# Performance work log

Hardware: AMD Instinct MI355X
Metric: run time of the kernel (lower is better)

## Reference

```python
import jax, jax.numpy as jnp
import numpy as np

B, S, D = 2, 2048, 2048
H, HK, HD = 16, 4, 128          # query heads, kv heads, head dim (H*HD == D)
HID = 4 * D                      # SwiGLU hidden (mult=4)
WIN, SINK = 1024, 4              # sliding window, attention sink tokens
EPS = 1e-6
ROPE_BASE = 10000.0


def rmsnorm(x, g):
    return x * jax.lax.rsqrt(jnp.mean(x * x, axis=-1, keepdims=True) + EPS) * g


def rope_tables(seq_len, head_dim):
    inv = 1.0 / (ROPE_BASE ** (jnp.arange(0, head_dim, 2, dtype=jnp.float32) / head_dim))
    ang = jnp.arange(seq_len, dtype=jnp.float32)[:, None] * inv[None, :]  # [S, HD/2]
    return jnp.cos(ang), jnp.sin(ang)


def apply_rope(x, cos, sin):
    # x: [B, S, h, HD]; rotate-half convention
    x1, x2 = jnp.split(x, 2, axis=-1)
    c = cos[None, :, None, :]
    s = sin[None, :, None, :]
    return jnp.concatenate([x1 * c - x2 * s, x2 * c + x1 * s], axis=-1)


def setup_inputs() -> dict:
    key = jax.random.key(0)
    ks = jax.random.split(key, 10)
    p = 0.02
    return {
        "x": jax.random.normal(ks[0], (B, S, D), dtype=jnp.float32),
        "g1": jnp.ones((D,), dtype=jnp.float32),
        "g2": jnp.ones((D,), dtype=jnp.float32),
        "wq": jax.random.normal(ks[1], (D, H * HD), dtype=jnp.float32) * p,
        "wk": jax.random.normal(ks[2], (D, HK * HD), dtype=jnp.float32) * p,
        "wv": jax.random.normal(ks[3], (D, HK * HD), dtype=jnp.float32) * p,
        "wo": jax.random.normal(ks[4], (H * HD, D), dtype=jnp.float32) * p,
        "w_gate": jax.random.normal(ks[5], (D, HID), dtype=jnp.float32) * p,
        "w_up": jax.random.normal(ks[6], (D, HID), dtype=jnp.float32) * p,
        "w_down": jax.random.normal(ks[7], (HID, D), dtype=jnp.float32) * p,
    }


def reference(x, g1, g2, wq, wk, wv, wo, w_gate, w_up, w_down):
    # ---- pre-norm attention ----
    h = rmsnorm(x, g1)
    q = (h @ wq).reshape(B, S, H, HD)
    k = (h @ wk).reshape(B, S, HK, HD)
    v = (h @ wv).reshape(B, S, HK, HD)

    cos, sin = rope_tables(S, HD)
    q = apply_rope(q, cos, sin)
    k = apply_rope(k, cos, sin)

    # GQA: expand kv heads to query heads
    rep = H // HK
    k = jnp.repeat(k, rep, axis=2)  # [B, S, H, HD]
    v = jnp.repeat(v, rep, axis=2)

    scores = jnp.einsum("bqhd,bkhd->bhqk", q, k) / jnp.sqrt(jnp.float32(HD))

    # causal + sliding-window + attention-sink mask
    i = jnp.arange(S)[:, None]
    j = jnp.arange(S)[None, :]
    allowed = (j <= i) & (((i - j) < WIN) | (j < SINK))  # [S, S]
    scores = jnp.where(allowed[None, None], scores, jnp.float32(-1e9))

    attn = jax.nn.softmax(scores, axis=-1)
    a = jnp.einsum("bhqk,bkhd->bqhd", attn, v).reshape(B, S, H * HD) @ wo

    x = x + a

    # ---- pre-norm SwiGLU FFN ----
    h2 = rmsnorm(x, g2)
    ffn = (jax.nn.silu(h2 @ w_gate) * (h2 @ w_up)) @ w_down
    return x + ffn
```

## Files before the change

kernel.cpp:

```cpp
#include <hip/hip_runtime.h>
#include <hip/hip_bf16.h>
#include <stdint.h>

#define TOK 4096
#define SEQ 2048
#define DM 2048
#define NH 16
#define NKV 4
#define HDIM 128
#define HID 8192
#define WIN 1024
#define SINKN 4

typedef float f32x4 __attribute__((ext_vector_type(4)));
typedef __bf16 bf16x8 __attribute__((ext_vector_type(8)));
typedef unsigned short u16;
typedef unsigned int u32;

#define VM(n) asm volatile("s_waitcnt vmcnt(" #n ")" ::: "memory")
#define LG(n) asm volatile("s_waitcnt lgkmcnt(" #n ")" ::: "memory")
#define SCHED0 __builtin_amdgcn_sched_barrier(0)

__device__ __forceinline__ u16 f2bf(float f) {
  union { float f; u32 u; } v; v.f = f;
  return (u16)((v.u + 0x7fffu + ((v.u >> 16) & 1u)) >> 16);
}
__device__ __forceinline__ float bf2f(u16 h) {
  union { u32 u; float f; } v; v.u = ((u32)h) << 16;
  return v.f;
}
__device__ __forceinline__ f32x4 mfma16(bf16x8 a, bf16x8 b, f32x4 c) {
  return __builtin_amdgcn_mfma_f32_16x16x32_bf16(a, b, c, 0, 0, 0);
}
__device__ __forceinline__ void gld16(const u16* g, u16* l) {
  __builtin_amdgcn_global_load_lds(
      (const __attribute__((address_space(1))) u32*)g,
      (__attribute__((address_space(3))) u32*)l, 16, 0, 0);
}
__device__ __forceinline__ void bar() {
  asm volatile("s_barrier" ::: "memory");
}
__device__ __forceinline__ void swz_rc(int c, int& row, int& k8) {
  row = 2 * (c >> 3) + (((c >> 2) & 1) ^ ((c >> 4) & 1));
  k8 = (c & 3) ^ (row & 3);
}
__device__ __forceinline__ void raster8(int wg, int nwg, int nbx, int& bx, int& by) {
  int cpx = nwg >> 3;
  int s = (wg & 7) * cpx + (wg >> 3);
  by = 8 * (s / (8 * nbx)) + (s & 7);
  bx = (s >> 3) % nbx;
}

__global__ __launch_bounds__(256)
void wtrans_all(const float* __restrict__ wq, const float* __restrict__ wk,
                const float* __restrict__ wv, const float* __restrict__ wo,
                const float* __restrict__ wg, const float* __restrict__ wu,
                const float* __restrict__ wd,
                u16* __restrict__ dqkv, u16* __restrict__ dwo,
                u16* __restrict__ dwg, u16* __restrict__ dwu,
                u16* __restrict__ dwd)
{
  int id = blockIdx.x;
  const float* src; u16* dst; int K, N, lgn;
  if (id < 4096)       { src = wq; dst = dqkv;                        K = 2048; N = 2048; lgn = 6; }
  else if (id < 5120)  { id -= 4096;  src = wk; dst = dqkv + (size_t)DM * DM;          K = 2048; N = 512;  lgn = 4; }
  else if (id < 6144)  { id -= 5120;  src = wv; dst = dqkv + (size_t)(DM + 512) * DM;  K = 2048; N = 512;  lgn = 4; }
  else if (id < 10240) { id -= 6144;  src = wo; dst = dwo;            K = 2048; N = 2048; lgn = 6; }
  else if (id < 26624) { id -= 10240; src = wg; dst = dwg;            K = 2048; N = 8192; lgn = 8; }
  else if (id < 43008) { id -= 26624; src = wu; dst = dwu;            K = 2048; N = 8192; lgn = 8; }
  else                 { id -= 43008; src = wd; dst = dwd;            K = 8192; N = 2048; lgn = 6; }
  int bx = id & ((1 << lgn) - 1);
  int by = id >> lgn;

  __shared__ float t[32][33];
  int tx = threadIdx.x & 31, ty = threadIdx.x >> 5;
  #pragma unroll
  for (int i = 0; i < 4; i++) {
    int r = ty + i * 8;
    t[r][tx] = src[(size_t)(by * 32 + r) * N + bx * 32 + tx];
  }
  __syncthreads();
  #pragma unroll
  for (int i = 0; i < 4; i++) {
    int r = ty + i * 8;
    dst[(size_t)(bx * 32 + r) * K + by * 32 + tx] = f2bf(t[tx][r]);
  }
}

__global__ __launch_bounds__(256)
void vtrans(const u16* __restrict__ in, int ld, u16* __restrict__ out)
{
  __shared__ u16 t[32][33];
  int tx = threadIdx.x & 31, ty = threadIdx.x >> 5;
  int bx = blockIdx.x;
  int by = blockIdx.y;
  #pragma unroll
  for (int i = 0; i < 4; i++) {
    int r = ty + i * 8;
    t[r][tx] = in[(size_t)(by * 32 + r) * ld + bx * 32 + tx];
  }
  __syncthreads();
  int b = (by * 32) >> 11;
  int s0 = (by * 32) & (SEQ - 1);
  #pragma unroll
  for (int i = 0; i < 4; i++) {
    int c = bx * 32 + ty + i * 8;
    out[(size_t)(b * (NKV * HDIM) + c) * SEQ + s0 + tx] = t[tx][ty + i * 8];
  }
}

__global__ __launch_bounds__(256)
void rope_table_k(float* __restrict__ ct, float* __restrict__ st)
{
  int idx = blockIdx.x * 256 + threadIdx.x;
  int pos = idx >> 6, d = idx & 63;
  float inv = powf(10000.0f, -(float)d / 64.0f);
  float a = (float)pos * inv;
  ct[idx] = cosf(a);
  st[idx] = sinf(a);
}

__global__ void rope_apply_k(u16* __restrict__ q, int ld,
                             const float* __restrict__ ct,
                             const float* __restrict__ st, float scale)
{
  int t = blockIdx.x;
  int hh = threadIdx.x >> 6;
  int d = threadIdx.x & 63;
  int pos = t & (SEQ - 1);
  size_t base = (size_t)t * ld + hh * HDIM + d;
  float x1 = bf2f(q[base]), x2 = bf2f(q[base + 64]);
  float c = ct[pos * 64 + d], s = st[pos * 64 + d];
  q[base]      = f2bf((x1 * c - x2 * s) * scale);
  q[base + 64] = f2bf((x2 * c + x1 * s) * scale);
}

__global__ __launch_bounds__(256)
void rmsnorm_k(const float* __restrict__ x, const float* __restrict__ g,
               u16* __restrict__ o)
{
  int row = blockIdx.x;
  int tid = threadIdx.x;
  const float* xr = x + (size_t)row * DM;
  float4 v0 = *(const float4*)(xr + tid * 8);
  float4 v1 = *(const float4*)(xr + tid * 8 + 4);
  float ss = v0.x*v0.x + v0.y*v0.y + v0.z*v0.z + v0.w*v0.w
           + v1.x*v1.x + v1.y*v1.y + v1.z*v1.z + v1.w*v1.w;
  #pragma unroll
  for (int d = 1; d < 64; d <<= 1) ss += __shfl_xor(ss, d);
  __shared__ float red[4];
  if ((tid & 63) == 0) red[tid >> 6] = ss;
  __syncthreads();
  float inv = rsqrtf((red[0] + red[1] + red[2] + red[3]) * (1.0f / DM) + 1e-6f);
  float4 g0 = *(const float4*)(g + tid * 8);
  float4 g1 = *(const float4*)(g + tid * 8 + 4);
  ushort4 o0, o1;
  o0.x = f2bf(v0.x * inv * g0.x); o0.y = f2bf(v0.y * inv * g0.y);
  o0.z = f2bf(v0.z * inv * g0.z); o0.w = f2bf(v0.w * inv * g0.w);
  o1.x = f2bf(v1.x * inv * g1.x); o1.y = f2bf(v1.y * inv * g1.y);
  o1.z = f2bf(v1.z * inv * g1.z); o1.w = f2bf(v1.w * inv * g1.w);
  *(ushort4*)(o + (size_t)row * DM + tid * 8) = o0;
  *(ushort4*)(o + (size_t)row * DM + tid * 8 + 4) = o1;
}

template<int EPI>
__global__ __launch_bounds__(512, 1)
void gemmp(const u16* __restrict__ A, const u16* __restrict__ Bt,
           u16* __restrict__ Cb, float* __restrict__ Cf,
           const float* __restrict__ X, int M, int N, int K, int nbx)
{
  constexpr int ASZ = 128 * 64;
  constexpr int SLOT = ASZ + 256 * 64;
  __shared__ u16 lds[3 * SLOT];

  int bx, by;
  raster8(blockIdx.x, gridDim.x, nbx, bx, by);
  int m0 = by * 128;
  int n0 = bx * 256;

  int tid = threadIdx.x;
  int l = tid & 63, w = tid >> 6;
  int l16 = l & 15, lg = l >> 4;
  int wr = w >> 2, wc = w & 3;

  int aoff[4][2], boff[4][2];
  #pragma unroll
  for (int m = 0; m < 4; m++)
    #pragma unroll
    for (int kk = 0; kk < 2; kk++) {
      int row = wr * 64 + m * 16 + l16;
      aoff[m][kk] = ((row * 128 + kk * 64 + lg * 16) ^ ((row & 7) << 4)) >> 1;
    }
  #pragma unroll
  for (int n = 0; n < 4; n++)
    #pragma unroll
    for (int kk = 0; kk < 2; kk++) {
      int br = wc * 64 + n * 16 + l16;
      boff[n][kk] = ASZ + (((br * 128 + kk * 64 + lg * 16) ^ ((br & 7) << 4)) >> 1);
    }

  int urow = tid >> 3;
  int cc = (tid & 7) ^ (urow & 7);
  const u16* pA[2];
  const u16* pB[4];
  pA[0] = A + (size_t)(m0 + urow) * K + cc * 8;
  pA[1] = A + (size_t)(m0 + 64 + urow) * K + cc * 8;
  #pragma unroll
  for (int u = 0; u < 4; u++)
    pB[u] = Bt + (size_t)(n0 + u * 64 + urow) * K + cc * 8;

  const int NT = K >> 6;

  auto stA = [&](int tt, int u) {
    gld16(pA[u] + (size_t)tt * 64, lds + (tt % 3) * SLOT + u * 4096 + tid * 8);
  };
  auto stB = [&](int tt, int u) {
    gld16(pB[u] + (size_t)tt * 64, lds + (tt % 3) * SLOT + ASZ + u * 4096 + tid * 8);
  };

  #pragma unroll
  for (int u = 0; u < 4; u++) stB(0, u);
  stA(0, 0); stA(0, 1);
  #pragma unroll
  for (int u = 0; u < 4; u++) stB(1, u);
  stA(1, 0); stA(1, 1);
  VM(6);
  bar();

  f32x4 acc[4][4];
  f32x4 zero = {0.f, 0.f, 0.f, 0.f};
  #pragma unroll
  for (int m = 0; m < 4; m++)
    #pragma unroll
    for (int n = 0; n < 4; n++) acc[m][n] = zero;

  for (int t = 0; t < NT; ++t) {
    u16* cur = lds + (t % 3) * SLOT;
    const bool st = (t + 2 < NT);

    if (st) { stB(t + 2, 0); stB(t + 2, 1); stB(t + 2, 2); }
    bf16x8 a[4][2], b[2][2], c2[2][2];
    #pragma unroll
    for (int m = 0; m < 4; m++) {
      a[m][0] = *(const bf16x8*)(cur + aoff[m][0]);
      a[m][1] = *(const bf16x8*)(cur + aoff[m][1]);
    }
    #pragma unroll
    for (int n = 0; n < 2; n++) {
      b[n][0] = *(const bf16x8*)(cur + boff[n][0]);
      b[n][1] = *(const bf16x8*)(cur + boff[n][1]);
    }
    SCHED0;
    #pragma unroll
    for (int n = 0; n < 2; n++) {
      c2[n][0] = *(const bf16x8*)(cur + boff[n + 2][0]);
      c2[n][1] = *(const bf16x8*)(cur + boff[n + 2][1]);
    }
    bar();
    LG(4);
    SCHED0;
    __builtin_amdgcn_s_setprio(1);
    #pragma unroll
    for (int m = 0; m < 4; m++)
      #pragma unroll
      for (int n = 0; n < 2; n++) {
        acc[m][n] = mfma16(a[m][0], b[n][0], acc[m][n]);
        acc[m][n] = mfma16(a[m][1], b[n][1], acc[m][n]);
      }
    __builtin_amdgcn_s_setprio(0);
    SCHED0;
    bar();

    if (st) { stB(t + 2, 3); stA(t + 2, 0); stA(t + 2, 1); }
    if (st) { VM(6); }
    else if (t + 1 < NT) { VM(0); }
    bar();
    LG(0);
    SCHED0;
    __builtin_amdgcn_s_setprio(1);
    #pragma unroll
    for (int m = 0; m < 4; m++)
      #pragma unroll
      for (int n = 0; n < 2; n++) {
        acc[m][n + 2] = mfma16(a[m][0], c2[n][0], acc[m][n + 2]);
        acc[m][n + 2] = mfma16(a[m][1], c2[n][1], acc[m][n + 2]);
      }
    __builtin_amdgcn_s_setprio(0);
    SCHED0;
    bar();
  }

  #pragma unroll
  for (int m = 0; m < 4; m++) {
    int row = m0 + wr * 64 + m * 16 + lg * 4;
    #pragma unroll
    for (int n = 0; n < 4; n++) {
      int col = n0 + wc * 64 + n * 16 + l16;
      #pragma unroll
      for (int r = 0; r < 4; r++) {
        size_t idx = (size_t)(row + r) * N + col;
        float v = acc[m][n][r];
        if (EPI == 0) {
          Cb[idx] = f2bf(v);
        } else if (EPI == 1) {
          Cf[idx] = X[idx] + v;
        } else {
          Cf[idx] += v;
        }
      }
    }
  }
}

template<int EPI, int GU, int SPLITK>
__global__ __launch_bounds__(512, 1)
void gemm256(const u16* __restrict__ A, const u16* __restrict__ B1,
             const u16* __restrict__ B2, u16* __restrict__ Cb,
             float* __restrict__ Cf, int Kst, int NT, int N, int nbx)
{
  constexpr int SLOT = 32768;
  __shared__ u16 lds[2 * SLOT];

  int wg = blockIdx.x;
  int nwg = gridDim.x;
  int kh = 0;
  if (SPLITK) { int half = nwg >> 1; kh = (wg >= half); wg -= kh * half; nwg = half; }
  int bx, by;
  raster8(wg, nwg, nbx, bx, by);
  int m0 = by * 256;
  int n0 = bx * (GU ? 128 : 256);
  size_t k0 = (size_t)kh * NT * 64;

  int tid = threadIdx.x;
  int l = tid & 63, w = tid >> 6;
  int l16 = l & 15, lg = l >> 4;
  int wr = w >> 2, wc = w & 3;

  int aoff[4][2], boff[2][2];
  #pragma unroll
  for (int mm = 0; mm < 4; mm++)
    #pragma unroll
    for (int kk = 0; kk < 2; kk++) {
      int ar = wr * 64 + mm * 16 + l16;
      aoff[mm][kk] = ((ar * 128 + ((kk * 64 + lg * 16) ^ ((ar & 7) << 4))) >> 1);
    }
  #pragma unroll
  for (int nn = 0; nn < 2; nn++)
    #pragma unroll
    for (int kk = 0; kk < 2; kk++) {
      int br = wc * 32 + nn * 16 + l16;
      boff[nn][kk] = 16384 + ((br * 128 + ((kk * 64 + lg * 16) ^ ((br & 7) << 4))) >> 1);
    }

  int rh = tid >> 3;
  int cc = (tid & 7) ^ (rh & 7);
  const u16* pA[4];
  #pragma unroll
  for (int u = 0; u < 4; u++)
    pA[u] = A + (size_t)(m0 + u * 64 + rh) * Kst + k0 + cc * 8;
  const u16* pB[4];
  #pragma unroll
  for (int u = 0; u < 4; u++) {
    if (GU) pB[u] = (u < 2 ? B1 + (size_t)(n0 + u * 64 + rh) * Kst
                           : B2 + (size_t)(n0 + (u - 2) * 64 + rh) * Kst) + k0 + cc * 8;
    else    pB[u] = B1 + (size_t)(n0 + u * 64 + rh) * Kst + k0 + cc * 8;
  }

  auto stA = [&](int tt, int h) {
    u16* d = lds + (tt & 1) * SLOT + h * 8192;
    gld16(pA[h * 2 + 0] + (size_t)tt * 64, d + tid * 8);
    gld16(pA[h * 2 + 1] + (size_t)tt * 64, d + 4096 + tid * 8);
  };
  auto stB = [&](int tt, int h) {
    u16* d = lds + (tt & 1) * SLOT + 16384 + h * 8192;
    gld16(pB[h * 2 + 0] + (size_t)tt * 64, d + tid * 8);
    gld16(pB[h * 2 + 1] + (size_t)tt * 64, d + 4096 + tid * 8);
  };

  stA(0, 0); stB(0, 0); stA(0, 1); stB(0, 1);
  stA(1, 0); stB(1, 0); stA(1, 1);
  VM(6);
  bar();

  f32x4 acc[8][4];
  f32x4 zero = {0.f, 0.f, 0.f, 0.f};
  #pragma unroll
  for (int m = 0; m < 8; m++)
    #pragma unroll
    for (int n = 0; n < 4; n++) acc[m][n] = zero;

  #pragma unroll 2
  for (int t = 0; t < NT; ++t) {
    u16* cur = lds + (t & 1) * SLOT;
    bf16x8 a0[4][2], a1[4][2], b0[2][2], b1[2][2];

    #pragma unroll
    for (int mm = 0; mm < 4; mm++)
      #pragma unroll
      for (int kk = 0; kk < 2; kk++)
        a0[mm][kk] = *(const bf16x8*)(cur + aoff[mm][kk]);
    #pragma unroll
    for (int nn = 0; nn < 2; nn++)
      #pragma unroll
      for (int kk = 0; kk < 2; kk++)
        b0[nn][kk] = *(const bf16x8*)(cur + boff[nn][kk]);
    if (t + 1 < NT) stB(t + 1, 1);
    LG(8);
    bar();
    LG(0);
    SCHED0;
    __builtin_amdgcn_s_setprio(1);
    #pragma unroll
    for (int mm = 0; mm < 4; mm++)
      #pragma unroll
      for (int nn = 0; nn < 2; nn++)
        #pragma unroll
        for (int kk = 0; kk < 2; kk++)
          acc[mm][nn] = mfma16(a0[mm][kk], b0[nn][kk], acc[mm][nn]);
    __builtin_amdgcn_s_setprio(0);
    SCHED0;
    bar();

    #pragma unroll
    for (int nn = 0; nn < 2; nn++)
      #pragma unroll
      for (int kk = 0; kk < 2; kk++)
        b1[nn][kk] = *(const bf16x8*)(cur + boff[nn][kk] + 8192);
    if (t + 2 < NT) stA(t + 2, 0);
    bar();
    LG(0);
    SCHED0;
    __builtin_amdgcn_s_setprio(1);
    #pragma unroll
    for (int mm = 0; mm < 4; mm++)
      #pragma unroll
      for (int nn = 0; nn < 2; nn++)
        #pragma unroll
        for (int kk = 0; kk < 2; kk++)
          acc[mm][2 + nn] = mfma16(a0[mm][kk], b1[nn][kk], acc[mm][2 + nn]);
    __builtin_amdgcn_s_setprio(0);
    SCHED0;
    bar();

    #pragma unroll
    for (int mm = 0; mm < 4; mm++)
      #pragma unroll
      for (int kk = 0; kk < 2; kk++)
        a1[mm][kk] = *(const bf16x8*)(cur + aoff[mm][kk] + 8192);
    if (t + 2 < NT) stB(t + 2, 0);
    bar();
    LG(0);
    SCHED0;
    __builtin_amdgcn_s_setprio(1);
    #pragma unroll
    for (int mm = 0; mm < 4; mm++)
      #pragma unroll
      for (int nn = 0; nn < 2; nn++)
        #pragma unroll
        for (int kk = 0; kk < 2; kk++)
          acc[4 + mm][nn] = mfma16(a1[mm][kk], b0[nn][kk], acc[4 + mm][nn]);
    __builtin_amdgcn_s_setprio(0);
    SCHED0;
    bar();

    if (t + 2 < NT) { stA(t + 2, 1); VM(6); }
    else if (t + 1 < NT) { VM(0); }
    bar();
    SCHED0;
    __builtin_amdgcn_s_setprio(1);
    #pragma unroll
    for (int mm = 0; mm < 4; mm++)
      #pragma unroll
      for (int nn = 0; nn < 2; nn++)
        #pragma unroll
        for (int kk = 0; kk < 2; kk++)
          acc[4 + mm][2 + nn] = mfma16(a1[mm][kk], b1[nn][kk], acc[4 + mm][2 + nn]);
    __builtin_amdgcn_s_setprio(0);
    SCHED0;
    bar();
  }

  if (GU) {
    #pragma unroll
    for (int m = 0; m < 8; m++) {
      int row = m0 + (m >> 2) * 128 + wr * 64 + (m & 3) * 16 + lg * 4;
      #pragma unroll
      for (int nn = 0; nn < 2; nn++) {
        int col = n0 + wc * 32 + nn * 16 + l16;
        #pragma unroll
        for (int r = 0; r < 4; r++) {
          float gt = acc[m][nn][r];
          float up = acc[m][2 + nn][r];
          float sg = gt / (1.0f + __expf(-gt));
          Cb[(size_t)(row + r) * N + col] = f2bf(sg * up);
        }
      }
    }
  } else {
    #pragma unroll
    for (int m = 0; m < 8; m++) {
      int row = m0 + (m >> 2) * 128 + wr * 64 + (m & 3) * 16 + lg * 4;
      #pragma unroll
      for (int n = 0; n < 4; n++) {
        int col = n0 + (n >> 1) * 128 + wc * 32 + (n & 1) * 16 + l16;
        #pragma unroll
        for (int r = 0; r < 4; r++) {
          size_t idx = (size_t)(row + r) * N + col;
          if (EPI == 0) Cb[idx] = f2bf(acc[m][n][r]);
          else          atomicAdd(Cf + idx, acc[m][n][r]);
        }
      }
    }
  }
}

__global__ __launch_bounds__(256)
void attn_k(const u16* __restrict__ qb, int ldq,
            const u16* __restrict__ kb, int ldk,
            const u16* __restrict__ vbt, u16* __restrict__ ao,
            const float* __restrict__ ct, const float* __restrict__ st)
{
  int q0 = blockIdx.x * 128;
  int h = blockIdx.y;
  int b = blockIdx.z;
  int hk = h >> 2;
  int tid = threadIdx.x;
  int w = tid >> 6, l = tid & 63;
  int l16 = l & 15, lg = l >> 4;

  __shared__ u16 Ks[2][32 * 128];
  __shared__ u16 Vt[2][128 * 32];
  __shared__ u16 Ps[4][32 * 40];
  u16* Pw = Ps[w];

  const float qscale = 0.08838834764831845f;
  bf16x8 qf[2][4];
  #pragma unroll
  for (int m = 0; m < 2; m++) {
    int row = q0 + w * 32 + m * 16 + l16;
    #pragma unroll
    for (int kd = 0; kd < 4; kd++)
      qf[m][kd] = *(const bf16x8*)(qb + (size_t)(b * SEQ + row) * ldq
                                   + h * HDIM + kd * 32 + lg * 8);
    const float* ctp = ct + (size_t)row * 64;
    const float* stp = st + (size_t)row * 64;
    #pragma unroll
    for (int pr = 0; pr < 2; pr++) {
      bf16x8 lo = qf[m][pr], hi = qf[m][pr + 2];
      int dl = pr * 32 + lg * 8;
      #pragma unroll
      for (int j = 0; j < 8; j++) {
        float c = ctp[dl + j], s = stp[dl + j];
        float x1 = (float)lo[j], x2 = (float)hi[j];
        lo[j] = (__bf16)((x1 * c - x2 * s) * qscale);
        hi[j] = (__bf16)((x2 * c + x1 * s) * qscale);
      }
      qf[m][pr] = lo; qf[m][pr + 2] = hi;
    }
  }

  f32x4 oacc[2][8];
  float mrun[2][4], lrun[2][4];
  f32x4 zero = {0.f, 0.f, 0.f, 0.f};
  #pragma unroll
  for (int m = 0; m < 2; m++) {
    #pragma unroll
    for (int nd = 0; nd < 8; nd++) oacc[m][nd] = zero;
    #pragma unroll
    for (int r = 0; r < 4; r++) { mrun[m][r] = -1e9f; lrun[m][r] = 0.f; }
  }

  int kr0 = tid >> 4,        kc0 = (tid & 15) ^ (kr0 & 7);
  int kr1 = (tid + 256) >> 4, kc1 = (tid & 15) ^ (kr1 & 7);
  int vd0, vk0, vd1, vk1;
  swz_rc(tid, vd0, vk0);
  swz_rc(tid + 256, vd1, vk1);
  const u16* kbase = kb + (size_t)(b * SEQ) * ldk + hk * HDIM;
  const u16* vbase = vbt + (size_t)(b * NKV + hk) * HDIM * SEQ;

  int koff[2][4];
  #pragma unroll
  for (int n = 0; n < 2; n++)
    #pragma unroll
    for (int kd = 0; kd < 4; kd++) {
      int key = n * 16 + l16;
      koff[n][kd] = ((key * 128) + kd * 32 + lg * 8) ^ ((key & 7) * 8);
    }
  int voff[8];
  #pragma unroll
  for (int nd = 0; nd < 8; nd++) {
    int d = nd * 16 + l16;
    voff[nd] = (d * 32 + lg * 8) ^ ((d & 7) * 8);
  }

  auto stage = [&](int kt, int bsel) {
    gld16(kbase + (size_t)(kt * 32 + kr0) * ldk + kc0 * 8, Ks[bsel] + tid * 8);
    gld16(kbase + (size_t)(kt * 32 + kr1) * ldk + kc1 * 8, Ks[bsel] + (tid + 256) * 8);
    gld16(vbase + (size_t)vd0 * SEQ + kt * 32 + vk0 * 8, Vt[bsel] + tid * 8);
    gld16(vbase + (size_t)vd1 * SEQ + kt * 32 + vk1 * 8, Vt[bsel] + (tid + 256) * 8);
  };

  int lo = (q0 >= WIN) ? ((q0 - (WIN - 1)) >> 5) : 0;
  int hi = (q0 + 127) >> 5;
  int it0 = (lo > 0 ? lo - 1 : 0);

  stage((it0 < lo) ? 0 : it0, 0);
  int bsel = 0;

  for (int it = it0; it <= hi; ++it) {
    int kt = (it < lo) ? 0 : it;
    if (it < hi) { stage(it + 1, bsel ^ 1); VM(4); }
    else         { VM(0); }
    bar();
    const u16* Ksb = Ks[bsel];
    const u16* Vtb = Vt[bsel];

    f32x4 sacc[2][2];
    sacc[0][0] = zero; sacc[0][1] = zero; sacc[1][0] = zero; sacc[1][1] = zero;
    #pragma unroll
    for (int kd = 0; kd < 4; kd++) {
      bf16x8 kf0 = *(const bf16x8*)(Ksb + koff[0][kd]);
      bf16x8 kf1 = *(const bf16x8*)(Ksb + koff[1][kd]);
      #pragma unroll
      for (int m = 0; m < 2; m++) {
        sacc[m][0] = mfma16(qf[m][kd], kf0, sacc[m][0]);
        sacc[m][1] = mfma16(qf[m][kd], kf1, sacc[m][1]);
      }
    }

    #pragma unroll
    for (int m = 0; m < 2; m++) {
      float sc[4];
      #pragma unroll
      for (int r = 0; r < 4; r++) {
        int i = q0 + w * 32 + m * 16 + lg * 4 + r;
        int j0 = kt * 32 + l16;
        int j1 = j0 + 16;
        float s0 = sacc[m][0][r];
        float s1 = sacc[m][1][r];
        bool ok0 = (j0 <= i) && ((i - j0 < WIN) || (j0 < SINKN));
        bool ok1 = (j1 <= i) && ((i - j1 < WIN) || (j1 < SINKN));
        s0 = ok0 ? s0 : -1e9f;
        s1 = ok1 ? s1 : -1e9f;
        float mx = fmaxf(s0, s1);
        mx = fmaxf(mx, __shfl_xor(mx, 1));
        mx = fmaxf(mx, __shfl_xor(mx, 2));
        mx = fmaxf(mx, __shfl_xor(mx, 4));
        mx = fmaxf(mx, __shfl_xor(mx, 8));
        float mold = mrun[m][r];
        float mnew = fmaxf(mold, mx);
        float scl = __expf(mold - mnew);
        mrun[m][r] = mnew;
        float p0 = __expf(s0 - mnew);
        float p1 = __expf(s1 - mnew);
        int prow = m * 16 + lg * 4 + r;
        Pw[prow * 40 + l16] = f2bf(p0);
        Pw[prow * 40 + 16 + l16] = f2bf(p1);
        float ps = p0 + p1;
        ps += __shfl_xor(ps, 1);
        ps += __shfl_xor(ps, 2);
        ps += __shfl_xor(ps, 4);
        ps += __shfl_xor(ps, 8);
        lrun[m][r] = lrun[m][r] * scl + ps;
        sc[r] = scl;
      }
      #pragma unroll
      for (int nd = 0; nd < 8; nd++) {
        oacc[m][nd][0] *= sc[0];
        oacc[m][nd][1] *= sc[1];
        oacc[m][nd][2] *= sc[2];
        oacc[m][nd][3] *= sc[3];
      }
    }

    bf16x8 pa0 = *(const bf16x8*)(Pw + l16 * 40 + lg * 8);
    bf16x8 pa1 = *(const bf16x8*)(Pw + (16 + l16) * 40 + lg * 8);
    #pragma unroll
    for (int nd = 0; nd < 8; nd++) {
      bf16x8 vf = *(const bf16x8*)(Vtb + voff[nd]);
      oacc[0][nd] = mfma16(pa0, vf, oacc[0][nd]);
      oacc[1][nd] = mfma16(pa1, vf, oacc[1][nd]);
    }
    bar();
    bsel ^= 1;
  }

  #pragma unroll
  for (int m = 0; m < 2; m++)
    #pragma unroll
    for (int r = 0; r < 4; r++) {
      float invl = 1.0f / lrun[m][r];
      int row = q0 + w * 32 + m * 16 + lg * 4 + r;
      #pragma unroll
      for (int nd = 0; nd < 8; nd++) {
        int col = nd * 16 + l16;
        ao[(size_t)(b * SEQ + row) * (NH * HDIM) + h * HDIM + col] =
            f2bf(oacc[m][nd][r] * invl);
      }
    }
}

extern "C" void kernel_launch(void* const* d_in, const int* in_sizes, int n_in,
                              void* d_out, int out_size, void* d_ws, size_t ws_size,
                              hipStream_t stream)
{
  (void)in_sizes; (void)n_in; (void)out_size;
  const float* x  = (const float*)d_in[0];
  const float* g1 = (const float*)d_in[1];
  const float* g2 = (const float*)d_in[2];
  const float* wq = (const float*)d_in[3];
  const float* wk = (const float*)d_in[4];
  const float* wv = (const float*)d_in[5];
  const float* wo = (const float*)d_in[6];
  const float* wg = (const float*)d_in[7];
  const float* wu = (const float*)d_in[8];
  const float* wd = (const float*)d_in[9];
  float* out = (float*)d_out;

  char* ws = (char*)d_ws;
  size_t off = 0;
  auto alloc = [&](size_t bytes) {
    char* p = ws + off;
    off += (bytes + 255) & ~(size_t)255;
    return p;
  };
  const int NQKV = 3072;
  u16* wqkv_t = (u16*)alloc((size_t)NQKV * DM * 2);
  u16* wo_t   = (u16*)alloc((size_t)DM * DM * 2);
  u16* wg_t   = (u16*)alloc((size_t)HID * DM * 2);
  u16* wu_t   = (u16*)alloc((size_t)HID * DM * 2);
  u16* wd_t   = (u16*)alloc((size_t)DM * HID * 2);
  u16* hb     = (u16*)alloc((size_t)TOK * DM * 2);
  char* span0 = ws + off;
  u16* qkvb   = (u16*)alloc((size_t)TOK * NQKV * 2);
  u16* vbt    = (u16*)alloc((size_t)TOK * NKV * HDIM * 2);
  u16* aob    = (u16*)alloc((size_t)TOK * NH * HDIM * 2);
  size_t span_used = (size_t)(ws + off - span0);
  size_t gu_need = (size_t)TOK * HID * 2;
  if (gu_need > span_used) alloc(gu_need - span_used);
  u16* gu = (u16*)span0;
  float* ct  = (float*)alloc((size_t)SEQ * 64 * 4);
  float* st  = (float*)alloc((size_t)SEQ * 64 * 4);
  if (off > ws_size) return;

  dim3 blk(256);
  dim3 blk512(512);

  wtrans_all<<<dim3(59392), blk, 0, stream>>>(wq, wk, wv, wo, wg, wu, wd,
                                              wqkv_t, wo_t, wg_t, wu_t, wd_t);

  rope_table_k<<<SEQ * 64 / 256, blk, 0, stream>>>(ct, st);
  rmsnorm_k<<<TOK, blk, 0, stream>>>(x, g1, hb);

  gemm256<0, 0, 0><<<dim3((NQKV / 256) * (TOK / 256)), blk512, 0, stream>>>(
      hb, wqkv_t, nullptr, qkvb, nullptr, DM, DM / 64, NQKV, NQKV / 256);

  rope_apply_k<<<TOK, dim3(NKV * 64), 0, stream>>>(qkvb + DM, NQKV, ct, st, 1.0f);
  vtrans<<<dim3((NKV * HDIM) / 32, TOK / 32), blk, 0, stream>>>(qkvb + DM + NKV * HDIM, NQKV, vbt);

  attn_k<<<dim3(SEQ / 128, NH, 2), blk, 0, stream>>>(qkvb, NQKV, qkvb + DM, NQKV, vbt, aob, ct, st);

  gemmp<1><<<dim3((DM / 256) * (TOK / 128)), blk512, 0, stream>>>(
      aob, wo_t, nullptr, out, x, TOK, DM, DM, DM / 256);
  rmsnorm_k<<<TOK, blk, 0, stream>>>(out, g2, hb);

  gemm256<0, 1, 0><<<dim3((HID / 128) * (TOK / 256)), blk512, 0, stream>>>(
      hb, wg_t, wu_t, gu, nullptr, DM, DM / 64, HID, HID / 128);

  gemm256<4, 0, 1><<<dim3(2 * (DM / 256) * (TOK / 256)), blk512, 0, stream>>>(
      gu, wd_t, nullptr, nullptr, out, HID, HID / 128, DM, DM / 256);
}
```

Measured before the change: 736.8 us.

## Merge setup kernels, fuse K-rope with V transpose, trim GEMM barriers

Result: no change. 731.0 us (-0.8%).

```diff
diff --git a/kernel.cpp b/kernel.cpp
--- a/kernel.cpp
+++ b/kernel.cpp
@@ -52,15 +52,54 @@
 }
 
 __global__ __launch_bounds__(256)
-void wtrans_all(const float* __restrict__ wq, const float* __restrict__ wk,
-                const float* __restrict__ wv, const float* __restrict__ wo,
-                const float* __restrict__ wg, const float* __restrict__ wu,
-                const float* __restrict__ wd,
-                u16* __restrict__ dqkv, u16* __restrict__ dwo,
-                u16* __restrict__ dwg, u16* __restrict__ dwu,
-                u16* __restrict__ dwd)
+void setup_all(const float* __restrict__ wq, const float* __restrict__ wk,
+               const float* __restrict__ wv, const float* __restrict__ wo,
+               const float* __restrict__ wg, const float* __restrict__ wu,
+               const float* __restrict__ wd,
+               u16* __restrict__ dqkv, u16* __restrict__ dwo,
+               u16* __restrict__ dwg, u16* __restrict__ dwu,
+               u16* __restrict__ dwd,
+               float* __restrict__ ct, float* __restrict__ st,
+               const float* __restrict__ x, const float* __restrict__ g1,
+               u16* __restrict__ hb)
 {
   int id = blockIdx.x;
+  int tid = threadIdx.x;
+  __shared__ float t[32][33];
+
+  if (id >= 59904) {
+    int row = id - 59904;
+    const float* xr = x + (size_t)row * DM;
+    float4 v0 = *(const float4*)(xr + tid * 8);
+    float4 v1 = *(const float4*)(xr + tid * 8 + 4);
+    float ss = v0.x*v0.x + v0.y*v0.y + v0.z*v0.z + v0.w*v0.w
+             + v1.x*v1.x + v1.y*v1.y + v1.z*v1.z + v1.w*v1.w;
+    #pragma unroll
+    for (int d = 1; d < 64; d <<= 1) ss += __shfl_xor(ss, d);
+    float* red = &t[0][0];
+    if ((tid & 63) == 0) red[tid >> 6] = ss;
+    __syncthreads();
+    float inv = rsqrtf((red[0] + red[1] + red[2] + red[3]) * (1.0f / DM) + 1e-6f);
+    float4 q0 = *(const float4*)(g1 + tid * 8);
+    float4 q1 = *(const float4*)(g1 + tid * 8 + 4);
+    ushort4 o0, o1;
+    o0.x = f2bf(v0.x * inv * q0.x); o0.y = f2bf(v0.y * inv * q0.y);
+    o0.z = f2bf(v0.z * inv * q0.z); o0.w = f2bf(v0.w * inv * q0.w);
+    o1.x = f2bf(v1.x * inv * q1.x); o1.y = f2bf(v1.y * inv * q1.y);
+    o1.z = f2bf(v1.z * inv * q1.z); o1.w = f2bf(v1.w * inv * q1.w);
+    *(ushort4*)(hb + (size_t)row * DM + tid * 8) = o0;
+    *(ushort4*)(hb + (size_t)row * DM + tid * 8 + 4) = o1;
+    return;
+  }
+  if (id >= 59392) {
+    int idx = (id - 59392) * 256 + tid;
+    int pos = idx >> 6, d = idx & 63;
+    float inv = powf(10000.0f, -(float)d / 64.0f);
+    float a = (float)pos * inv;
+    ct[idx] = cosf(a);
+    st[idx] = sinf(a);
+    return;
+  }
   const float* src; u16* dst; int K, N, lgn;
   if (id < 4096)       { src = wq; dst = dqkv;                        K = 2048; N = 2048; lgn = 6; }
   else if (id < 5120)  { id -= 4096;  src = wk; dst = dqkv + (size_t)DM * DM;          K = 2048; N = 512;  lgn = 4; }
@@ -71,9 +110,7 @@
   else                 { id -= 43008; src = wd; dst = dwd;            K = 8192; N = 2048; lgn = 6; }
   int bx = id & ((1 << lgn) - 1);
   int by = id >> lgn;
-
-  __shared__ float t[32][33];
-  int tx = threadIdx.x & 31, ty = threadIdx.x >> 5;
+  int tx = tid & 31, ty = tid >> 5;
   #pragma unroll
   for (int i = 0; i < 4; i++) {
     int r = ty + i * 8;
@@ -88,16 +125,33 @@
 }
 
 __global__ __launch_bounds__(256)
-void vtrans(const u16* __restrict__ in, int ld, u16* __restrict__ out)
+void kv_post(u16* __restrict__ qkvb, const float* __restrict__ ct,
+             const float* __restrict__ st, u16* __restrict__ vbt)
 {
+  const int NQKV = 3072;
+  int id = blockIdx.x;
+  int tid = threadIdx.x;
+  if (id < 4096) {
+    int tt = id;
+    int hh = tid >> 6;
+    int d = tid & 63;
+    int pos = tt & (SEQ - 1);
+    size_t base = (size_t)tt * NQKV + DM + hh * HDIM + d;
+    float x1 = bf2f(qkvb[base]), x2 = bf2f(qkvb[base + 64]);
+    float c = ct[pos * 64 + d], s = st[pos * 64 + d];
+    qkvb[base]      = f2bf(x1 * c - x2 * s);
+    qkvb[base + 64] = f2bf(x2 * c + x1 * s);
+    return;
+  }
+  id -= 4096;
+  int bx = id & 15, by = id >> 4;
+  const u16* in = qkvb + DM + NKV * HDIM;
   __shared__ u16 t[32][33];
-  int tx = threadIdx.x & 31, ty = threadIdx.x >> 5;
-  int bx = blockIdx.x;
-  int by = blockIdx.y;
+  int tx = tid & 31, ty = tid >> 5;
   #pragma unroll
   for (int i = 0; i < 4; i++) {
     int r = ty + i * 8;
-    t[r][tx] = in[(size_t)(by * 32 + r) * ld + bx * 32 + tx];
+    t[r][tx] = in[(size_t)(by * 32 + r) * NQKV + bx * 32 + tx];
   }
   __syncthreads();
   int b = (by * 32) >> 11;
@@ -105,34 +159,8 @@
   #pragma unroll
   for (int i = 0; i < 4; i++) {
     int c = bx * 32 + ty + i * 8;
-    out[(size_t)(b * (NKV * HDIM) + c) * SEQ + s0 + tx] = t[tx][ty + i * 8];
-  }
-}
-
-__global__ __launch_bounds__(256)
-void rope_table_k(float* __restrict__ ct, float* __restrict__ st)
-{
-  int idx = blockIdx.x * 256 + threadIdx.x;
-  int pos = idx >> 6, d = idx & 63;
-  float inv = powf(10000.0f, -(float)d / 64.0f);
-  float a = (float)pos * inv;
-  ct[idx] = cosf(a);
-  st[idx] = sinf(a);
-}
-
-__global__ void rope_apply_k(u16* __restrict__ q, int ld,
-                             const float* __restrict__ ct,
-                             const float* __restrict__ st, float scale)
-{
-  int t = blockIdx.x;
-  int hh = threadIdx.x >> 6;
-  int d = threadIdx.x & 63;
-  int pos = t & (SEQ - 1);
-  size_t base = (size_t)t * ld + hh * HDIM + d;
-  float x1 = bf2f(q[base]), x2 = bf2f(q[base + 64]);
-  float c = ct[pos * 64 + d], s = st[pos * 64 + d];
-  q[base]      = f2bf((x1 * c - x2 * s) * scale);
-  q[base + 64] = f2bf((x2 * c + x1 * s) * scale);
+    vbt[(size_t)(b * (NKV * HDIM) + c) * SEQ + s0 + tx] = t[tx][ty + i * 8];
+  }
 }
 
 __global__ __launch_bounds__(256)
@@ -379,7 +407,7 @@
 
   stA(0, 0); stB(0, 0); stA(0, 1); stB(0, 1);
   stA(1, 0); stB(1, 0); stA(1, 1);
-  VM(6);
+  VM(8);
   bar();
 
   f32x4 acc[8][4];
@@ -404,10 +432,10 @@
       #pragma unroll
       for (int kk = 0; kk < 2; kk++)
         b0[nn][kk] = *(const bf16x8*)(cur + boff[nn][kk]);
+    LG(0);
+    if (t + 1 < NT) { VM(6); } else { VM(0); }
+    bar();
     if (t + 1 < NT) stB(t + 1, 1);
-    LG(8);
-    bar();
-    LG(0);
     SCHED0;
     __builtin_amdgcn_s_setprio(1);
     #pragma unroll
@@ -419,16 +447,15 @@
           acc[mm][nn] = mfma16(a0[mm][kk], b0[nn][kk], acc[mm][nn]);
     __builtin_amdgcn_s_setprio(0);
     SCHED0;
-    bar();
 
     #pragma unroll
     for (int nn = 0; nn < 2; nn++)
       #pragma unroll
       for (int kk = 0; kk < 2; kk++)
         b1[nn][kk] = *(const bf16x8*)(cur + boff[nn][kk] + 8192);
+    LG(0);
+    bar();
     if (t + 2 < NT) stA(t + 2, 0);
-    bar();
-    LG(0);
     SCHED0;
     __builtin_amdgcn_s_setprio(1);
     #pragma unroll
@@ -440,16 +467,15 @@
           acc[mm][2 + nn] = mfma16(a0[mm][kk], b1[nn][kk], acc[mm][2 + nn]);
     __builtin_amdgcn_s_setprio(0);
     SCHED0;
-    bar();
 
     #pragma unroll
     for (int mm = 0; mm < 4; mm++)
       #pragma unroll
       for (int kk = 0; kk < 2; kk++)
         a1[mm][kk] = *(const bf16x8*)(cur + aoff[mm][kk] + 8192);
+    LG(0);
+    bar();
     if (t + 2 < NT) stB(t + 2, 0);
-    bar();
-    LG(0);
     SCHED0;
     __builtin_amdgcn_s_setprio(1);
     #pragma unroll
@@ -461,11 +487,10 @@
           acc[4 + mm][nn] = mfma16(a1[mm][kk], b0[nn][kk], acc[4 + mm][nn]);
     __builtin_amdgcn_s_setprio(0);
     SCHED0;
-    bar();
-
-    if (t + 2 < NT) { stA(t + 2, 1); VM(6); }
-    else if (t + 1 < NT) { VM(0); }
-    bar();
+
+    if (t + 2 < NT) { VM(8); } else { VM(0); }
+    bar();
+    if (t + 2 < NT) stA(t + 2, 1);
     SCHED0;
     __builtin_amdgcn_s_setprio(1);
     #pragma unroll
@@ -477,7 +502,6 @@
           acc[4 + mm][2 + nn] = mfma16(a1[mm][kk], b1[nn][kk], acc[4 + mm][2 + nn]);
     __builtin_amdgcn_s_setprio(0);
     SCHED0;
-    bar();
   }
 
   if (GU) {
@@ -746,17 +770,14 @@
   dim3 blk(256);
   dim3 blk512(512);
 
-  wtrans_all<<<dim3(59392), blk, 0, stream>>>(wq, wk, wv, wo, wg, wu, wd,
-                                              wqkv_t, wo_t, wg_t, wu_t, wd_t);
-
-  rope_table_k<<<SEQ * 64 / 256, blk, 0, stream>>>(ct, st);
-  rmsnorm_k<<<TOK, blk, 0, stream>>>(x, g1, hb);
+  setup_all<<<dim3(64000), blk, 0, stream>>>(wq, wk, wv, wo, wg, wu, wd,
+                                             wqkv_t, wo_t, wg_t, wu_t, wd_t,
+                                             ct, st, x, g1, hb);
 
   gemm256<0, 0, 0><<<dim3((NQKV / 256) * (TOK / 256)), blk512, 0, stream>>>(
       hb, wqkv_t, nullptr, qkvb, nullptr, DM, DM / 64, NQKV, NQKV / 256);
 
-  rope_apply_k<<<TOK, dim3(NKV * 64), 0, stream>>>(qkvb + DM, NQKV, ct, st, 1.0f);
-  vtrans<<<dim3((NKV * HDIM) / 32, TOK / 32), blk, 0, stream>>>(qkvb + DM + NKV * HDIM, NQKV, vbt);
+  kv_post<<<dim3(6144), blk, 0, stream>>>(qkvb, ct, st, vbt);
 
   attn_k<<<dim3(SEQ / 128, NH, 2), blk, 0, stream>>>(qkvb, NQKV, qkvb + DM, NQKV, vbt, aob, ct, st);
 
```
